# Performance work log

Hardware: AMD Instinct MI355X
Metric: run time of the kernel (lower is better)

Reference implementation:

```python
import jax, jax.numpy as jnp
import numpy as np

B = 4          # batch
C_FEAT = 32    # shared feature channels
N_PARTS = 24   # body parts
H = 256        # triplane resolution (W = 3*H, three planes concatenated on width)
N_PTS = 8192   # sampled points per batch element
C = C_FEAT + N_PARTS


def setup_inputs() -> dict:
    key = jax.random.key(0)
    k1, k2 = jax.random.split(key)
    triplane = jax.random.normal(k1, (B, C, H, 3 * H), dtype=jnp.float32)
    # canonical coords in [-1, 1], one row per (point, part)
    triplane_coord_3d = jax.random.uniform(
        k2, (B * N_PTS * N_PARTS, 3), dtype=jnp.float32, minval=-1.0, maxval=1.0)
    index = jnp.arange(B * N_PTS, dtype=jnp.int32).reshape(B, N_PTS)
    return {"triplane": triplane, "triplane_coord_3d": triplane_coord_3d, "index": index}


def _bilinear(planes, uv):
    """planes: (B, 3, C, H, H); uv: (B, P, 3, 2) in [-1,1] (x->width, y->height).
    align_corners=False, border-clamped bilinear sample. Returns (B, P, 3, C)."""
    Hs = planes.shape[-1]
    px = (uv[..., 0] + 1.0) * (Hs * 0.5) - 0.5
    py = (uv[..., 1] + 1.0) * (Hs * 0.5) - 0.5
    x0f = jnp.floor(px)
    y0f = jnp.floor(py)
    wx = px - x0f
    wy = py - y0f
    x0 = jnp.clip(x0f.astype(jnp.int32), 0, Hs - 1)
    x1 = jnp.clip(x0f.astype(jnp.int32) + 1, 0, Hs - 1)
    y0 = jnp.clip(y0f.astype(jnp.int32), 0, Hs - 1)
    y1 = jnp.clip(y0f.astype(jnp.int32) + 1, 0, Hs - 1)
    bi = jnp.arange(planes.shape[0])[:, None, None]   # (B,1,1)
    ki = jnp.arange(3)[None, None, :]                 # (1,1,3)

    def g(yi, xi):
        return planes[bi, ki, :, yi, xi]              # (B, P, 3, C)

    return (g(y0, x0) * ((1 - wx) * (1 - wy))[..., None]
            + g(y0, x1) * (wx * (1 - wy))[..., None]
            + g(y1, x0) * ((1 - wx) * wy)[..., None]
            + g(y1, x1) * (wx * wy)[..., None])


def reference(triplane, triplane_coord_3d, index):
    Bq, n = index.shape
    # split width into the 3 concatenated planes -> (B, 3, C, H, H)
    planes = triplane.reshape(Bq, C, H, 3, H).transpose(0, 3, 1, 2, 4)
    # per-(point, part) coordinate rows
    rows = index[..., None] * N_PARTS + jnp.arange(N_PARTS, dtype=index.dtype)  # (B,n,P)
    xyz = triplane_coord_3d[rows]                                 # (B, n, P, 3)
    # plane uv: xy, xz, yz
    uv = jnp.stack([xyz[..., jnp.array([0, 1])],
                    xyz[..., jnp.array([0, 2])],
                    xyz[..., jnp.array([1, 2])]], axis=-2)        # (B, n, P, 3, 2)
    uv = uv.reshape(Bq, n * N_PARTS, 3, 2)
    samp = _bilinear(planes, uv).sum(axis=2)                      # sum over 3 planes -> (B, nP, C)
    samp = samp.reshape(Bq, n, N_PARTS, C)
    part_feature = samp[..., :C_FEAT].mean(axis=-1)               # (B, n, P)
    # part p's probability logit is channel 32+p sampled at part p's coords
    logits = samp[:, :, jnp.arange(N_PARTS), C_FEAT + jnp.arange(N_PARTS)]
    part_prob = jax.nn.softmax(logits, axis=-1)                   # (B, n, P)
    return (part_prob * part_feature).sum(axis=-1)                # (B, n)
```

## Files before the change

kernel.cpp:

```cpp
#include <hip/hip_runtime.h>

#define HS 256
#define W3 768
#define CCH 56
#define CF 32
#define NP 24
#define NPTS 8192
#define PLANE_SZ (HS * W3)

__global__ void tp_mean_kernel(const float* __restrict__ tri,
                               float* __restrict__ M) {
    int i4 = blockIdx.x * blockDim.x + threadIdx.x;
    int b = i4 / (PLANE_SZ / 4);
    int rem = i4 % (PLANE_SZ / 4);
    const float4* in = (const float4*)tri + (size_t)b * CCH * (PLANE_SZ / 4) + rem;
    float4 acc = {0.f, 0.f, 0.f, 0.f};
#pragma unroll
    for (int c = 0; c < CF; ++c) {
        float4 v = in[(size_t)c * (PLANE_SZ / 4)];
        acc.x += v.x; acc.y += v.y; acc.z += v.z; acc.w += v.w;
    }
    const float s = 1.0f / (float)CF;
    acc.x *= s; acc.y *= s; acc.z *= s; acc.w *= s;
    ((float4*)M)[(size_t)b * (PLANE_SZ / 4) + rem] = acc;
}

__global__ __launch_bounds__(192) void tp_sample_kernel(
    const float* __restrict__ tri, const float* __restrict__ coords,
    const int* __restrict__ index, const float* __restrict__ M,
    float* __restrict__ out) {
    __shared__ float s_feat[8][NP];
    __shared__ float s_log[8][NP];

    const int tid = threadIdx.x;
    const int lp = tid / NP;
    const int part = tid % NP;
    const int point = blockIdx.x * 8 + lp;
    const int b = point >> 13;

    const int idx = index[point];
    const int row = idx * NP + part;
    const float x = coords[row * 3 + 0];
    const float y = coords[row * 3 + 1];
    const float z = coords[row * 3 + 2];

    const float us[3] = {x, x, y};
    const float vs[3] = {y, z, z};

    const float* __restrict__ Mb = M + (size_t)b * PLANE_SZ;
    const float* __restrict__ Tb = tri + (size_t)(b * CCH + CF + part) * PLANE_SZ;

    float feat = 0.f, lg = 0.f;
#pragma unroll
    for (int k = 0; k < 3; ++k) {
        const float px = (us[k] + 1.0f) * (HS * 0.5f) - 0.5f;
        const float py = (vs[k] + 1.0f) * (HS * 0.5f) - 0.5f;
        const float x0f = floorf(px);
        const float y0f = floorf(py);
        const float wx = px - x0f;
        const float wy = py - y0f;
        const int x0 = min(max((int)x0f, 0), HS - 1);
        const int x1 = min(max((int)x0f + 1, 0), HS - 1);
        const int y0 = min(max((int)y0f, 0), HS - 1);
        const int y1 = min(max((int)y0f + 1, 0), HS - 1);
        const float w00 = (1.f - wx) * (1.f - wy);
        const float w01 = wx * (1.f - wy);
        const float w10 = (1.f - wx) * wy;
        const float w11 = wx * wy;
        const int o00 = y0 * W3 + k * HS + x0;
        const int o01 = y0 * W3 + k * HS + x1;
        const int o10 = y1 * W3 + k * HS + x0;
        const int o11 = y1 * W3 + k * HS + x1;
        feat += Mb[o00] * w00 + Mb[o01] * w01 + Mb[o10] * w10 + Mb[o11] * w11;
        lg   += Tb[o00] * w00 + Tb[o01] * w01 + Tb[o10] * w10 + Tb[o11] * w11;
    }

    s_feat[lp][part] = feat;
    s_log[lp][part] = lg;
    __syncthreads();

    if (tid < 8) {
        float mx = -1e30f;
#pragma unroll
        for (int j = 0; j < NP; ++j) mx = fmaxf(mx, s_log[tid][j]);
        float se = 0.f, acc = 0.f;
#pragma unroll
        for (int j = 0; j < NP; ++j) {
            const float e = __expf(s_log[tid][j] - mx);
            se += e;
            acc += e * s_feat[tid][j];
        }
        out[blockIdx.x * 8 + tid] = acc / se;
    }
}

extern "C" void kernel_launch(void* const* d_in, const int* in_sizes, int n_in,
                              void* d_out, int out_size, void* d_ws, size_t ws_size,
                              hipStream_t stream) {
    const float* tri = (const float*)d_in[0];
    const float* coords = (const float*)d_in[1];
    const int* index = (const int*)d_in[2];
    float* out = (float*)d_out;
    float* M = (float*)d_ws;

    tp_mean_kernel<<<(4 * PLANE_SZ / 4) / 256, 256, 0, stream>>>(tri, M);

    tp_sample_kernel<<<4096, 192, 0, stream>>>(tri, coords, index, M, out);
}
```

Before: 308.6 us.

## Remap blocks per XCD by batch, pair texel loads, transpose thread-part mapping

Blocks are remapped so that each of the eight XCDs (block id mod 8) handles half of one batch element. This is meant to keep that batch's planes in one XCD's L2 and improve cache locality. Horizontally adjacent bilinear taps are fetched with one float2 load when aligned, and an odd x0 falls back to a scalar load. Threads are now ordered part-major, so the 8 lanes for consecutive points share a part and its logit channel plane. This adds branchy load code and relies on round-robin XCD dispatch.

```diff
diff --git a/kernel.cpp b/kernel.cpp
--- a/kernel.cpp
+++ b/kernel.cpp
@@ -25,18 +25,37 @@
     ((float4*)M)[(size_t)b * (PLANE_SZ / 4) + rem] = acc;
 }
 
+__device__ __forceinline__ void sample_row(const float* __restrict__ row,
+                                           int x0, int x1,
+                                           float& c0, float& c1) {
+    const int xa = x0 & ~1;
+    const float2 v = *reinterpret_cast<const float2*>(row + xa);
+    if (x0 & 1) {
+        c0 = v.y;
+        c1 = (x1 == x0) ? v.y : row[x1];
+    } else {
+        c0 = v.x;
+        c1 = (x1 == x0) ? v.x : v.y;
+    }
+}
+
 __global__ __launch_bounds__(192) void tp_sample_kernel(
     const float* __restrict__ tri, const float* __restrict__ coords,
     const int* __restrict__ index, const float* __restrict__ M,
     float* __restrict__ out) {
-    __shared__ float s_feat[8][NP];
-    __shared__ float s_log[8][NP];
+    __shared__ float s_feat[NP][8];
+    __shared__ float s_log[NP][8];
 
     const int tid = threadIdx.x;
-    const int lp = tid / NP;
-    const int part = tid % NP;
-    const int point = blockIdx.x * 8 + lp;
-    const int b = point >> 13;
+    const int part = tid >> 3;
+    const int lp = tid & 7;
+
+    const int xcd = blockIdx.x & 7;
+    const int slot = blockIdx.x >> 3;
+    const int b = xcd >> 1;
+    const int chunk = ((xcd & 1) << 9) + slot;
+    const int point_base = b * NPTS + chunk * 8;
+    const int point = point_base + lp;
 
     const int idx = index[point];
     const int row = idx * NP + part;
@@ -59,38 +78,46 @@
         const float y0f = floorf(py);
         const float wx = px - x0f;
         const float wy = py - y0f;
-        const int x0 = min(max((int)x0f, 0), HS - 1);
-        const int x1 = min(max((int)x0f + 1, 0), HS - 1);
-        const int y0 = min(max((int)y0f, 0), HS - 1);
-        const int y1 = min(max((int)y0f + 1, 0), HS - 1);
+        const int x0i = (int)x0f;
+        const int y0i = (int)y0f;
+        const int x0 = min(max(x0i, 0), HS - 1);
+        const int x1 = min(max(x0i + 1, 0), HS - 1);
+        const int y0 = min(max(y0i, 0), HS - 1);
+        const int y1 = min(max(y0i + 1, 0), HS - 1);
         const float w00 = (1.f - wx) * (1.f - wy);
         const float w01 = wx * (1.f - wy);
         const float w10 = (1.f - wx) * wy;
         const float w11 = wx * wy;
-        const int o00 = y0 * W3 + k * HS + x0;
-        const int o01 = y0 * W3 + k * HS + x1;
-        const int o10 = y1 * W3 + k * HS + x0;
-        const int o11 = y1 * W3 + k * HS + x1;
-        feat += Mb[o00] * w00 + Mb[o01] * w01 + Mb[o10] * w10 + Mb[o11] * w11;
-        lg   += Tb[o00] * w00 + Tb[o01] * w01 + Tb[o10] * w10 + Tb[o11] * w11;
+
+        const int r0 = y0 * W3 + k * HS;
+        const int r1 = y1 * W3 + k * HS;
+
+        float m00, m01, m10, m11, t00, t01, t10, t11;
+        sample_row(Mb + r0, x0, x1, m00, m01);
+        sample_row(Mb + r1, x0, x1, m10, m11);
+        sample_row(Tb + r0, x0, x1, t00, t01);
+        sample_row(Tb + r1, x0, x1, t10, t11);
+
+        feat += m00 * w00 + m01 * w01 + m10 * w10 + m11 * w11;
+        lg   += t00 * w00 + t01 * w01 + t10 * w10 + t11 * w11;
     }
 
-    s_feat[lp][part] = feat;
-    s_log[lp][part] = lg;
+    s_feat[part][lp] = feat;
+    s_log[part][lp] = lg;
     __syncthreads();
 
     if (tid < 8) {
         float mx = -1e30f;
 #pragma unroll
-        for (int j = 0; j < NP; ++j) mx = fmaxf(mx, s_log[tid][j]);
+        for (int j = 0; j < NP; ++j) mx = fmaxf(mx, s_log[j][tid]);
         float se = 0.f, acc = 0.f;
 #pragma unroll
         for (int j = 0; j < NP; ++j) {
-            const float e = __expf(s_log[tid][j] - mx);
+            const float e = __expf(s_log[j][tid] - mx);
             se += e;
-            acc += e * s_feat[tid][j];
+            acc += e * s_feat[j][tid];
         }
-        out[blockIdx.x * 8 + tid] = acc / se;
+        out[point_base + tid] = acc / se;
     }
 }
 
@@ -104,6 +131,5 @@
     float* M = (float*)d_ws;
 
     tp_mean_kernel<<<(4 * PLANE_SZ / 4) / 256, 256, 0, stream>>>(tri, M);
-
     tp_sample_kernel<<<4096, 192, 0, stream>>>(tri, coords, index, M, out);
 }
```

Measured after the change: 333.8 us. 8.2% more time.
